# Kernel tuning notes

Measured on AMD Instinct MI355X. Metric: run time of the kernel, lower is better.

## Reference

```python
import jax, jax.numpy as jnp
import numpy as np

T_END = 100.0
EPS = 1e-10
N_MC = 15
BATCH, MAXLEN, HIDDEN = 16, 384, 128


def _mlp(x, W1, b1, W2, b2, W3, b3, W4, b4):
    # x: [..., 1] -> [..., 1]; three tanh hidden layers + softplus head
    h = jnp.tanh(x @ W1 + b1)
    h = jnp.tanh(h @ W2 + b2)
    h = jnp.tanh(h @ W3 + b3)
    return jax.nn.softplus(h @ W4 + b4)


def setup_inputs() -> dict:
    key = jax.random.key(0)
    ks = jax.random.split(key, 6)
    # sorted event times in [0, T_END], zero-padded past seq_len
    times = jnp.sort(jax.random.uniform(ks[0], (BATCH, MAXLEN)) * T_END, axis=1)
    seq_lens = jax.random.randint(ks[1], (BATCH,), 1, MAXLEN + 1)
    valid = jnp.arange(MAXLEN)[None, :] < seq_lens[:, None]
    seq_pads = jnp.where(valid, times, 0.0)[..., None]

    def lin(k, fi, fo):
        bound = 1.0 / np.sqrt(fi)
        kw, kb = jax.random.split(k)
        W = jax.random.uniform(kw, (fi, fo), minval=-bound, maxval=bound)
        b = jax.random.uniform(kb, (fo,), minval=-bound, maxval=bound)
        return W, b

    W1, b1 = lin(ks[2], 1, HIDDEN)
    W2, b2 = lin(ks[3], HIDDEN, HIDDEN)
    W3, b3 = lin(ks[4], HIDDEN, HIDDEN)
    W4, b4 = lin(ks[5], HIDDEN, 1)
    background = jnp.ones((1,))
    return {"seq_pads": seq_pads, "seq_lens": seq_lens, "background": background,
            "W1": W1, "b1": b1, "W2": W2, "b2": b2,
            "W3": W3, "b3": b3, "W4": W4, "b4": b4}


def reference(seq_pads, seq_lens, background, W1, b1, W2, b2, W3, b3, W4, b4):
    batch, maxlen, _ = seq_pads.shape
    t = seq_pads[..., 0]                                   # [B, L]
    # all strictly-lower-triangular pair differences t_i - t_j (j < i), static indices
    r, c = np.tril_indices(maxlen - 1)
    i_idx = r + 1                                          # event index i in 1..L-1
    diffs = t[:, i_idx] - t[:, c]                          # [B, P], P = L*(L-1)/2
    lamb_pairs = _mlp(diffs[..., None], W1, b1, W2, b2, W3, b3, W4, b4)[..., 0]  # [B, P]
    # sum over j < i for each i -> lambs[b, i]; i = 0 gets 0
    lambs = jax.ops.segment_sum(lamb_pairs.T, jnp.asarray(i_idx), num_segments=maxlen).T
    lambs = lambs + background                             # [B, L]

    valid = jnp.arange(maxlen)[None, :] < seq_lens[:, None]
    diff_last = jnp.where(valid, T_END - t, 0.0)           # [B, L]

    # Monte Carlo integral of f over [t_i, T_END], 15 samples
    u = jax.random.uniform(jax.random.key(42), (N_MC, batch, maxlen))
    rand_time = u * diff_last                              # [S, B, L]
    lamb_samples = _mlp(rand_time[..., None], W1, b1, W2, b2, W3, b3, W4, b4)[..., 0] + EPS
    lamb_ints = (lamb_samples * diff_last).mean(0).sum(-1) + T_END * background  # [B]

    sum_log = jnp.where(valid, jnp.log(lambs), 0.0).sum()
    nll = -(sum_log - lamb_ints.sum()) / batch
    return nll
```

## Files before the change

### kernel.cpp

```cpp
#include <hip/hip_runtime.h>
#include <math.h>

#define T_END_F 100.0f
#define N_TAB 4096
#define HID 128
#define EVB 8
#define EVW 2
#define NBLK_TAB (N_TAB / EVB)
#define N_MC_TOTAL 92160
#define TF_HALF 46080u
#define FUSED_BLOCKS 512
#define NSLOT 16

__device__ __forceinline__ float softplusf(float z){
  return fmaxf(z, 0.0f) + log1pf(expf(-fabsf(z)));
}

__device__ __forceinline__ unsigned rotl32(unsigned x, unsigned d){
  return (x << d) | (x >> (32u - d));
}

__device__ float threefry_u01(unsigned idx){
  unsigned i0, i1;
  bool second = idx >= TF_HALF;
  if (second){ i0 = idx - TF_HALF; i1 = idx; }
  else       { i0 = idx;           i1 = idx + TF_HALF; }
  const unsigned ks0 = 0u;
  const unsigned ks1 = 42u;
  const unsigned ks2 = 0x1BD11BDAu ^ ks0 ^ ks1;
  unsigned x0 = i0 + ks0;
  unsigned x1 = i1 + ks1;
#define TF_R(r) { x0 += x1; x1 = rotl32(x1, (r)); x1 ^= x0; }
  TF_R(13) TF_R(15) TF_R(26) TF_R(6)
  x0 += ks1; x1 += ks2 + 1u;
  TF_R(17) TF_R(29) TF_R(16) TF_R(24)
  x0 += ks2; x1 += ks0 + 2u;
  TF_R(13) TF_R(15) TF_R(26) TF_R(6)
  x0 += ks0; x1 += ks1 + 3u;
  TF_R(17) TF_R(29) TF_R(16) TF_R(24)
  x0 += ks1; x1 += ks2 + 4u;
  TF_R(13) TF_R(15) TF_R(26) TF_R(6)
  x0 += ks2; x1 += ks0 + 5u;
#undef TF_R
  unsigned bits = second ? x1 : x0;
  unsigned fb = (bits >> 9) | 0x3F800000u;
  return __uint_as_float(fb) - 1.0f;
}

__device__ __forceinline__ float table_f(const float* __restrict__ tab, float x){
  float pos = x * ((float)(N_TAB - 1) / T_END_F);
  int i = (int)pos;
  if (i < 0) i = 0;
  if (i > N_TAB - 2) i = N_TAB - 2;
  float fr = pos - (float)i;
  float a = tab[i];
  float b = tab[i + 1];
  return fmaf(fr, b - a, a);
}

__device__ __forceinline__ void dense_tanh_layer(
    const float (*__restrict__ hin)[HID], float (*__restrict__ hout)[HID],
    const float* __restrict__ W, const float* __restrict__ bv,
    int k0, int k1, int ebase)
{
  float acc0[EVW], acc1[EVW];
  {
    float ba = bv[k0], bb = bv[k1];
#pragma unroll
    for (int e = 0; e < EVW; ++e){ acc0[e] = ba; acc1[e] = bb; }
  }
#pragma unroll 4
  for (int j = 0; j < HID; j += 4){
    float wa0 = W[(j+0)*HID + k0];
    float wa1 = W[(j+1)*HID + k0];
    float wa2 = W[(j+2)*HID + k0];
    float wa3 = W[(j+3)*HID + k0];
    float wb0 = W[(j+0)*HID + k1];
    float wb1 = W[(j+1)*HID + k1];
    float wb2 = W[(j+2)*HID + k1];
    float wb3 = W[(j+3)*HID + k1];
#pragma unroll
    for (int e = 0; e < EVW; ++e){
      float4 h = *(const float4*)&hin[ebase + e][j];
      float a0 = acc0[e], a1 = acc1[e];
      a0 = fmaf(h.x, wa0, a0); a1 = fmaf(h.x, wb0, a1);
      a0 = fmaf(h.y, wa1, a0); a1 = fmaf(h.y, wb1, a1);
      a0 = fmaf(h.z, wa2, a0); a1 = fmaf(h.z, wb2, a1);
      a0 = fmaf(h.w, wa3, a0); a1 = fmaf(h.w, wb3, a1);
      acc0[e] = a0; acc1[e] = a1;
    }
  }
#pragma unroll
  for (int e = 0; e < EVW; ++e){
    hout[ebase + e][k0] = tanhf(acc0[e]);
    hout[ebase + e][k1] = tanhf(acc1[e]);
  }
}

__global__ __launch_bounds__(256) void build_table_kernel(
    const float* __restrict__ W1, const float* __restrict__ b1v,
    const float* __restrict__ W2, const float* __restrict__ b2v,
    const float* __restrict__ W3, const float* __restrict__ b3v,
    const float* __restrict__ W4, const float* __restrict__ b4v,
    float* __restrict__ tab, float* __restrict__ slots, int* __restrict__ cnt)
{
  __shared__ float hA[EVB][HID];
  __shared__ float hB[EVB][HID];
  const int tid  = threadIdx.x;
  const int wv   = tid >> 6;
  const int lane = tid & 63;
  const int k0 = lane, k1 = lane + 64;
  const int ebase = wv * EVW;
  const int base = blockIdx.x * EVB;
  const float dt = T_END_F / (float)(N_TAB - 1);

  if (blockIdx.x == 0 && tid < 2 * NSLOT + 1){
    if (tid < 2 * NSLOT) slots[tid] = 0.0f;
    else *cnt = 0;
  }

  {
    float wa = W1[k0], wb = W1[k1];
    float ba = b1v[k0], bb = b1v[k1];
#pragma unroll
    for (int e = 0; e < EVW; ++e){
      float x = (float)(base + ebase + e) * dt;
      hA[ebase + e][k0] = tanhf(fmaf(x, wa, ba));
      hA[ebase + e][k1] = tanhf(fmaf(x, wb, bb));
    }
  }
  dense_tanh_layer(hA, hB, W2, b2v, k0, k1, ebase);
  dense_tanh_layer(hB, hA, W3, b3v, k0, k1, ebase);
  {
    float wa = W4[k0], wb = W4[k1];
    float b4s = b4v[0];
#pragma unroll
    for (int e = 0; e < EVW; ++e){
      float p = hA[ebase + e][k0] * wa + hA[ebase + e][k1] * wb;
      p += __shfl_xor(p, 32);
      p += __shfl_xor(p, 16);
      p += __shfl_xor(p, 8);
      p += __shfl_xor(p, 4);
      p += __shfl_xor(p, 2);
      p += __shfl_xor(p, 1);
      if (lane == 0) tab[base + ebase + e] = softplusf(p + b4s);
    }
  }
}

__global__ __launch_bounds__(256) void fused_kernel(
    const float* __restrict__ t,
    const int* __restrict__ seq_lens,
    const float* __restrict__ bg,
    const float* __restrict__ tab,
    float* __restrict__ slots,
    int* __restrict__ cnt,
    float* __restrict__ out)
{
  const int tid  = threadIdx.x;
  const int lane = tid & 63;
  const int wv   = tid >> 6;
  const int gwave = blockIdx.x * 4 + wv;
  const float bgv = bg[0];

  float logsum = 0.0f;
  float mcv    = 0.0f;

#pragma unroll
  for (int k = 0; k < 3; ++k){
    unsigned task = (unsigned)gwave + (unsigned)k * 2048u;
    unsigned b = task / 384u;
    int i = (int)(task - b * 384u);
    if (i < seq_lens[b]){
      const float* tb = t + b * 384u;
      float ti = tb[i];
      float s = 0.0f;
      for (int j = lane; j < i; j += 64)
        s += table_f(tab, ti - tb[j]);
      s += __shfl_xor(s, 32);
      s += __shfl_xor(s, 16);
      s += __shfl_xor(s, 8);
      s += __shfl_xor(s, 4);
      s += __shfl_xor(s, 2);
      s += __shfl_xor(s, 1);
      if (lane == 0) logsum += logf(s + bgv);
    }
  }

  {
    int idx = blockIdx.x * 256 + tid;
    if (idx < N_MC_TOTAL){
      int l = idx % 384;
      int b = (idx / 384) & 15;
      if (l < seq_lens[b]){
        float tv = t[b * 384 + l];
        float dl = T_END_F - tv;
        float u  = threefry_u01((unsigned)idx);
        mcv = (table_f(tab, u * dl) + 1e-10f) * dl;
      }
    }
  }
  mcv += __shfl_xor(mcv, 32);
  mcv += __shfl_xor(mcv, 16);
  mcv += __shfl_xor(mcv, 8);
  mcv += __shfl_xor(mcv, 4);
  mcv += __shfl_xor(mcv, 2);
  mcv += __shfl_xor(mcv, 1);

  __shared__ float redL[4], redM[4];
  if (lane == 0){ redL[wv] = logsum; redM[wv] = mcv; }
  __syncthreads();
  if (tid == 0){
    float bl = redL[0] + redL[1] + redL[2] + redL[3];
    float bm = redM[0] + redM[1] + redM[2] + redM[3];
    int slot = blockIdx.x & (NSLOT - 1);
    atomicAdd(&slots[slot], bl);
    atomicAdd(&slots[NSLOT + slot], bm);
    __threadfence();
    int old = atomicAdd(cnt, 1);
    if (old == (int)gridDim.x - 1){
      float sl = 0.0f, sm = 0.0f;
      for (int q = 0; q < NSLOT; ++q){
        sl += atomicAdd(&slots[q], 0.0f);
        sm += atomicAdd(&slots[NSLOT + q], 0.0f);
      }
      float lamb_ints_total = sm * (1.0f / 15.0f) + 16.0f * T_END_F * bgv;
      out[0] = -(sl - lamb_ints_total) / 16.0f;
    }
  }
}

extern "C" void kernel_launch(void* const* d_in, const int* in_sizes, int n_in,
                              void* d_out, int out_size, void* d_ws, size_t ws_size,
                              hipStream_t stream)
{
  const float* seq_pads = (const float*)d_in[0];
  const int*   seq_lens = (const int*)d_in[1];
  const float* bg       = (const float*)d_in[2];
  const float* W1 = (const float*)d_in[3];
  const float* b1 = (const float*)d_in[4];
  const float* W2 = (const float*)d_in[5];
  const float* b2 = (const float*)d_in[6];
  const float* W3 = (const float*)d_in[7];
  const float* b3 = (const float*)d_in[8];
  const float* W4 = (const float*)d_in[9];
  const float* b4 = (const float*)d_in[10];
  float* out = (float*)d_out;

  float* tab   = (float*)d_ws;
  float* slots = tab + N_TAB;
  int*   cnt   = (int*)(slots + 2 * NSLOT);

  build_table_kernel<<<NBLK_TAB, 256, 0, stream>>>(W1, b1, W2, b2, W3, b3, W4, b4,
                                                   tab, slots, cnt);
  fused_kernel<<<FUSED_BLOCKS, 256, 0, stream>>>(seq_pads, seq_lens, bg, tab,
                                                 slots, cnt, out);
}
```

Baseline: 112.9 us.

## Fuse table build and NLL evaluation into one cooperative kernel with LDS table

Merges the MLP table-building kernel and the pair-sum/Monte Carlo kernel into a single cooperative launch, separated by a grid-wide sync. After the sync each block copies the 4096-entry table into shared memory, and interpolation lookups read from LDS instead of global memory. The aim is to remove one kernel launch boundary and the global-memory gather latency. The cost is a grid-sync barrier and 16KB+ more LDS per block, and it relies on all 512 blocks being co-resident. If the cooperative launch fails, it falls back to the old two-kernel path.

```diff
diff --git a/kernel.cpp b/kernel.cpp
--- a/kernel.cpp
+++ b/kernel.cpp
@@ -1,5 +1,8 @@
 #include <hip/hip_runtime.h>
+#include <hip/hip_cooperative_groups.h>
 #include <math.h>
+
+namespace cg = cooperative_groups;
 
 #define T_END_F 100.0f
 #define N_TAB 4096
@@ -58,6 +61,16 @@
   return fmaf(fr, b - a, a);
 }
 
+#define TABLE_LDS(xval) ({                                        \
+  float _pos = (xval) * ((float)(N_TAB - 1) / T_END_F);           \
+  int _i = (int)_pos;                                             \
+  if (_i < 0) _i = 0;                                             \
+  if (_i > N_TAB - 2) _i = N_TAB - 2;                             \
+  float _fr = _pos - (float)_i;                                   \
+  float _a = sm_tab[_i];                                          \
+  float _b = sm_tab[_i + 1];                                      \
+  fmaf(_fr, _b - _a, _a); })
+
 __device__ __forceinline__ void dense_tanh_layer(
     const float (*__restrict__ hin)[HID], float (*__restrict__ hout)[HID],
     const float* __restrict__ W, const float* __restrict__ bv,
@@ -94,6 +107,145 @@
   for (int e = 0; e < EVW; ++e){
     hout[ebase + e][k0] = tanhf(acc0[e]);
     hout[ebase + e][k1] = tanhf(acc1[e]);
+  }
+}
+
+__global__ __launch_bounds__(256) void mc_nll_fused(
+    const float* __restrict__ W1, const float* __restrict__ b1v,
+    const float* __restrict__ W2, const float* __restrict__ b2v,
+    const float* __restrict__ W3, const float* __restrict__ b3v,
+    const float* __restrict__ W4, const float* __restrict__ b4v,
+    const float* __restrict__ t,
+    const int* __restrict__ seq_lens,
+    const float* __restrict__ bg,
+    float* __restrict__ tab,
+    float* __restrict__ slots,
+    int* __restrict__ cnt,
+    float* __restrict__ out)
+{
+  __shared__ float hA[EVB][HID];
+  __shared__ float hB[EVB][HID];
+  __shared__ float sm_tab[N_TAB];
+  __shared__ float redL[4], redM[4];
+
+  const int tid  = threadIdx.x;
+  const int wv   = tid >> 6;
+  const int lane = tid & 63;
+  const int k0 = lane, k1 = lane + 64;
+  const int ebase = wv * EVW;
+  const int base = blockIdx.x * EVB;
+  const float dt = T_END_F / (float)(N_TAB - 1);
+
+  if (blockIdx.x == 0 && tid < 2 * NSLOT + 1){
+    if (tid < 2 * NSLOT) slots[tid] = 0.0f;
+    else *cnt = 0;
+  }
+
+  {
+    float wa = W1[k0], wb = W1[k1];
+    float ba = b1v[k0], bb = b1v[k1];
+#pragma unroll
+    for (int e = 0; e < EVW; ++e){
+      float x = (float)(base + ebase + e) * dt;
+      hA[ebase + e][k0] = tanhf(fmaf(x, wa, ba));
+      hA[ebase + e][k1] = tanhf(fmaf(x, wb, bb));
+    }
+  }
+  dense_tanh_layer(hA, hB, W2, b2v, k0, k1, ebase);
+  dense_tanh_layer(hB, hA, W3, b3v, k0, k1, ebase);
+  {
+    float wa = W4[k0], wb = W4[k1];
+    float b4s = b4v[0];
+#pragma unroll
+    for (int e = 0; e < EVW; ++e){
+      float p = hA[ebase + e][k0] * wa + hA[ebase + e][k1] * wb;
+      p += __shfl_xor(p, 32);
+      p += __shfl_xor(p, 16);
+      p += __shfl_xor(p, 8);
+      p += __shfl_xor(p, 4);
+      p += __shfl_xor(p, 2);
+      p += __shfl_xor(p, 1);
+      if (lane == 0) tab[base + ebase + e] = softplusf(p + b4s);
+    }
+  }
+
+  cg::this_grid().sync();
+
+  {
+    const float4* g4 = (const float4*)tab;
+    float4* s4 = (float4*)sm_tab;
+#pragma unroll
+    for (int q = 0; q < (N_TAB / 4) / 256; ++q)
+      s4[q * 256 + tid] = g4[q * 256 + tid];
+  }
+  __syncthreads();
+
+  const float bgv = bg[0];
+  const int gwave = blockIdx.x * 4 + wv;
+
+  float logsum = 0.0f;
+  float mcv    = 0.0f;
+
+#pragma unroll
+  for (int k = 0; k < 3; ++k){
+    unsigned task = (unsigned)gwave + (unsigned)k * 2048u;
+    unsigned b = task / 384u;
+    int i = (int)(task - b * 384u);
+    if (i < seq_lens[b]){
+      const float* tb = t + b * 384u;
+      float ti = tb[i];
+      float s = 0.0f;
+      for (int j = lane; j < i; j += 64)
+        s += TABLE_LDS(ti - tb[j]);
+      s += __shfl_xor(s, 32);
+      s += __shfl_xor(s, 16);
+      s += __shfl_xor(s, 8);
+      s += __shfl_xor(s, 4);
+      s += __shfl_xor(s, 2);
+      s += __shfl_xor(s, 1);
+      if (lane == 0) logsum += logf(s + bgv);
+    }
+  }
+
+  {
+    int idx = blockIdx.x * 256 + tid;
+    if (idx < N_MC_TOTAL){
+      int l = idx % 384;
+      int b = (idx / 384) & 15;
+      if (l < seq_lens[b]){
+        float tv = t[b * 384 + l];
+        float dl = T_END_F - tv;
+        float u  = threefry_u01((unsigned)idx);
+        mcv = (TABLE_LDS(u * dl) + 1e-10f) * dl;
+      }
+    }
+  }
+  mcv += __shfl_xor(mcv, 32);
+  mcv += __shfl_xor(mcv, 16);
+  mcv += __shfl_xor(mcv, 8);
+  mcv += __shfl_xor(mcv, 4);
+  mcv += __shfl_xor(mcv, 2);
+  mcv += __shfl_xor(mcv, 1);
+
+  if (lane == 0){ redL[wv] = logsum; redM[wv] = mcv; }
+  __syncthreads();
+  if (tid == 0){
+    float bl = redL[0] + redL[1] + redL[2] + redL[3];
+    float bm = redM[0] + redM[1] + redM[2] + redM[3];
+    int slot = blockIdx.x & (NSLOT - 1);
+    atomicAdd(&slots[slot], bl);
+    atomicAdd(&slots[NSLOT + slot], bm);
+    __threadfence();
+    int old = atomicAdd(cnt, 1);
+    if (old == (int)gridDim.x - 1){
+      float sl = 0.0f, sm = 0.0f;
+      for (int q = 0; q < NSLOT; ++q){
+        sl += atomicAdd(&slots[q], 0.0f);
+        sm += atomicAdd(&slots[NSLOT + q], 0.0f);
+      }
+      float lamb_ints_total = sm * (1.0f / 15.0f) + 16.0f * T_END_F * bgv;
+      out[0] = -(sl - lamb_ints_total) / 16.0f;
+    }
   }
 }
 
@@ -251,8 +403,19 @@
   float* slots = tab + N_TAB;
   int*   cnt   = (int*)(slots + 2 * NSLOT);
 
-  build_table_kernel<<<NBLK_TAB, 256, 0, stream>>>(W1, b1, W2, b2, W3, b3, W4, b4,
-                                                   tab, slots, cnt);
-  fused_kernel<<<FUSED_BLOCKS, 256, 0, stream>>>(seq_pads, seq_lens, bg, tab,
-                                                 slots, cnt, out);
-}
+  void* args[] = {
+    (void*)&W1, (void*)&b1, (void*)&W2, (void*)&b2,
+    (void*)&W3, (void*)&b3, (void*)&W4, (void*)&b4,
+    (void*)&seq_pads, (void*)&seq_lens, (void*)&bg,
+    (void*)&tab, (void*)&slots, (void*)&cnt, (void*)&out
+  };
+  hipError_t err = hipLaunchCooperativeKernel(
+      reinterpret_cast<void*>(mc_nll_fused), dim3(FUSED_BLOCKS), dim3(256),
+      args, 0, stream);
+  if (err != hipSuccess){
+    build_table_kernel<<<NBLK_TAB, 256, 0, stream>>>(W1, b1, W2, b2, W3, b3, W4, b4,
+                                                     tab, slots, cnt);
+    fused_kernel<<<FUSED_BLOCKS, 256, 0, stream>>>(seq_pads, seq_lens, bg, tab,
+                                                   slots, cnt, out);
+  }
+}
```

New measurement: 162.4 us. 1.44x slower.

## Restructure table build, stage lookup table in LDS, spread fused work across more blocks

Applied to the files above, without the earlier changes.

The table-building kernel now uses 512-thread blocks covering 4 events each, with one hidden unit per thread and block barriers between layers. Before, each wave computed two units for two events. The fused kernel copies the 4096-entry table into shared memory once per block, so lookups read from LDS instead of global memory. It also launches 1536 blocks with one pair-sum task per wave instead of three per wave. The intent is more parallelism and cheaper table lookups. The cost is a 16 KB LDS copy per block, extra barriers, and more blocks taking part in the atomic reduction.

```diff
diff --git a/kernel.cpp b/kernel.cpp
--- a/kernel.cpp
+++ b/kernel.cpp
@@ -4,13 +4,15 @@
 #define T_END_F 100.0f
 #define N_TAB 4096
 #define HID 128
-#define EVB 8
-#define EVW 2
-#define NBLK_TAB (N_TAB / EVB)
 #define N_MC_TOTAL 92160
 #define TF_HALF 46080u
-#define FUSED_BLOCKS 512
 #define NSLOT 16
+
+#define B_EV 4
+#define B_THREADS 512
+#define NBLK_BUILD (N_TAB / B_EV)
+
+#define FUSED_BLOCKS 1536
 
 __device__ __forceinline__ float softplusf(float z){
   return fmaxf(z, 0.0f) + log1pf(expf(-fabsf(z)));
@@ -47,71 +49,46 @@
   return __uint_as_float(fb) - 1.0f;
 }
 
-__device__ __forceinline__ float table_f(const float* __restrict__ tab, float x){
-  float pos = x * ((float)(N_TAB - 1) / T_END_F);
-  int i = (int)pos;
-  if (i < 0) i = 0;
-  if (i > N_TAB - 2) i = N_TAB - 2;
-  float fr = pos - (float)i;
-  float a = tab[i];
-  float b = tab[i + 1];
-  return fmaf(fr, b - a, a);
-}
-
-__device__ __forceinline__ void dense_tanh_layer(
-    const float (*__restrict__ hin)[HID], float (*__restrict__ hout)[HID],
-    const float* __restrict__ W, const float* __restrict__ bv,
-    int k0, int k1, int ebase)
-{
-  float acc0[EVW], acc1[EVW];
-  {
-    float ba = bv[k0], bb = bv[k1];
-#pragma unroll
-    for (int e = 0; e < EVW; ++e){ acc0[e] = ba; acc1[e] = bb; }
-  }
+#define TABLE_LDS(xval) ({                                        \
+  float _pos = (xval) * ((float)(N_TAB - 1) / T_END_F);           \
+  int _i = (int)_pos;                                             \
+  if (_i < 0) _i = 0;                                             \
+  if (_i > N_TAB - 2) _i = N_TAB - 2;                             \
+  float _fr = _pos - (float)_i;                                   \
+  float _a = sm_tab[_i];                                          \
+  float _b = sm_tab[_i + 1];                                      \
+  fmaf(_fr, _b - _a, _a); })
+
+__device__ __forceinline__ float dense_dot(
+    const float* __restrict__ hrow,
+    const float* __restrict__ W,
+    int k, float bias)
+{
+  float acc = bias;
 #pragma unroll 4
   for (int j = 0; j < HID; j += 4){
-    float wa0 = W[(j+0)*HID + k0];
-    float wa1 = W[(j+1)*HID + k0];
-    float wa2 = W[(j+2)*HID + k0];
-    float wa3 = W[(j+3)*HID + k0];
-    float wb0 = W[(j+0)*HID + k1];
-    float wb1 = W[(j+1)*HID + k1];
-    float wb2 = W[(j+2)*HID + k1];
-    float wb3 = W[(j+3)*HID + k1];
-#pragma unroll
-    for (int e = 0; e < EVW; ++e){
-      float4 h = *(const float4*)&hin[ebase + e][j];
-      float a0 = acc0[e], a1 = acc1[e];
-      a0 = fmaf(h.x, wa0, a0); a1 = fmaf(h.x, wb0, a1);
-      a0 = fmaf(h.y, wa1, a0); a1 = fmaf(h.y, wb1, a1);
-      a0 = fmaf(h.z, wa2, a0); a1 = fmaf(h.z, wb2, a1);
-      a0 = fmaf(h.w, wa3, a0); a1 = fmaf(h.w, wb3, a1);
-      acc0[e] = a0; acc1[e] = a1;
-    }
-  }
-#pragma unroll
-  for (int e = 0; e < EVW; ++e){
-    hout[ebase + e][k0] = tanhf(acc0[e]);
-    hout[ebase + e][k1] = tanhf(acc1[e]);
-  }
-}
-
-__global__ __launch_bounds__(256) void build_table_kernel(
+    float4 h = *(const float4*)&hrow[j];
+    acc = fmaf(h.x, W[(j+0)*HID + k], acc);
+    acc = fmaf(h.y, W[(j+1)*HID + k], acc);
+    acc = fmaf(h.z, W[(j+2)*HID + k], acc);
+    acc = fmaf(h.w, W[(j+3)*HID + k], acc);
+  }
+  return acc;
+}
+
+__global__ __launch_bounds__(B_THREADS) void build_table_kernel(
     const float* __restrict__ W1, const float* __restrict__ b1v,
     const float* __restrict__ W2, const float* __restrict__ b2v,
     const float* __restrict__ W3, const float* __restrict__ b3v,
     const float* __restrict__ W4, const float* __restrict__ b4v,
     float* __restrict__ tab, float* __restrict__ slots, int* __restrict__ cnt)
 {
-  __shared__ float hA[EVB][HID];
-  __shared__ float hB[EVB][HID];
-  const int tid  = threadIdx.x;
-  const int wv   = tid >> 6;
-  const int lane = tid & 63;
-  const int k0 = lane, k1 = lane + 64;
-  const int ebase = wv * EVW;
-  const int base = blockIdx.x * EVB;
+  __shared__ float hA[B_EV][HID];
+  __shared__ float hB[B_EV][HID];
+  const int tid = threadIdx.x;
+  const int e   = tid >> 7;
+  const int k   = tid & 127;
+  const int base = blockIdx.x * B_EV;
   const float dt = T_END_F / (float)(N_TAB - 1);
 
   if (blockIdx.x == 0 && tid < 2 * NSLOT + 1){
@@ -120,30 +97,32 @@
   }
 
   {
-    float wa = W1[k0], wb = W1[k1];
-    float ba = b1v[k0], bb = b1v[k1];
-#pragma unroll
-    for (int e = 0; e < EVW; ++e){
-      float x = (float)(base + ebase + e) * dt;
-      hA[ebase + e][k0] = tanhf(fmaf(x, wa, ba));
-      hA[ebase + e][k1] = tanhf(fmaf(x, wb, bb));
-    }
-  }
-  dense_tanh_layer(hA, hB, W2, b2v, k0, k1, ebase);
-  dense_tanh_layer(hB, hA, W3, b3v, k0, k1, ebase);
-  {
-    float wa = W4[k0], wb = W4[k1];
-    float b4s = b4v[0];
-#pragma unroll
-    for (int e = 0; e < EVW; ++e){
-      float p = hA[ebase + e][k0] * wa + hA[ebase + e][k1] * wb;
+    float x = (float)(base + e) * dt;
+    hA[e][k] = tanhf(fmaf(x, W1[k], b1v[k]));
+  }
+  __syncthreads();
+
+  hB[e][k] = tanhf(dense_dot(hA[e], W2, k, b2v[k]));
+  __syncthreads();
+
+  hA[e][k] = tanhf(dense_dot(hB[e], W3, k, b3v[k]));
+  __syncthreads();
+
+  {
+    const int wv   = tid >> 6;
+    const int lane = tid & 63;
+    if ((wv & 1) == 0){
+      const int ee = wv >> 1;
+      float wa = W4[lane], wb = W4[lane + 64];
+      float b4s = b4v[0];
+      float p = hA[ee][lane] * wa + hA[ee][lane + 64] * wb;
       p += __shfl_xor(p, 32);
       p += __shfl_xor(p, 16);
       p += __shfl_xor(p, 8);
       p += __shfl_xor(p, 4);
       p += __shfl_xor(p, 2);
       p += __shfl_xor(p, 1);
-      if (lane == 0) tab[base + ebase + e] = softplusf(p + b4s);
+      if (lane == 0) tab[base + ee] = softplusf(p + b4s);
     }
   }
 }
@@ -157,18 +136,28 @@
     int* __restrict__ cnt,
     float* __restrict__ out)
 {
+  __shared__ float sm_tab[N_TAB];
+  __shared__ float redL[4], redM[4];
+
   const int tid  = threadIdx.x;
   const int lane = tid & 63;
   const int wv   = tid >> 6;
-  const int gwave = blockIdx.x * 4 + wv;
   const float bgv = bg[0];
+
+  {
+    const float4* g4 = (const float4*)tab;
+    float4* s4 = (float4*)sm_tab;
+#pragma unroll
+    for (int q = 0; q < 4; ++q)
+      s4[q * 256 + tid] = g4[q * 256 + tid];
+  }
+  __syncthreads();
 
   float logsum = 0.0f;
   float mcv    = 0.0f;
 
-#pragma unroll
-  for (int k = 0; k < 3; ++k){
-    unsigned task = (unsigned)gwave + (unsigned)k * 2048u;
+  {
+    unsigned task = (unsigned)(blockIdx.x * 4 + wv);
     unsigned b = task / 384u;
     int i = (int)(task - b * 384u);
     if (i < seq_lens[b]){
@@ -176,14 +165,14 @@
       float ti = tb[i];
       float s = 0.0f;
       for (int j = lane; j < i; j += 64)
-        s += table_f(tab, ti - tb[j]);
+        s += TABLE_LDS(ti - tb[j]);
       s += __shfl_xor(s, 32);
       s += __shfl_xor(s, 16);
       s += __shfl_xor(s, 8);
       s += __shfl_xor(s, 4);
       s += __shfl_xor(s, 2);
       s += __shfl_xor(s, 1);
-      if (lane == 0) logsum += logf(s + bgv);
+      if (lane == 0) logsum = logf(s + bgv);
     }
   }
 
@@ -196,7 +185,7 @@
         float tv = t[b * 384 + l];
         float dl = T_END_F - tv;
         float u  = threefry_u01((unsigned)idx);
-        mcv = (table_f(tab, u * dl) + 1e-10f) * dl;
+        mcv = (TABLE_LDS(u * dl) + 1e-10f) * dl;
       }
     }
   }
@@ -207,7 +196,6 @@
   mcv += __shfl_xor(mcv, 2);
   mcv += __shfl_xor(mcv, 1);
 
-  __shared__ float redL[4], redM[4];
   if (lane == 0){ redL[wv] = logsum; redM[wv] = mcv; }
   __syncthreads();
   if (tid == 0){
@@ -251,8 +239,8 @@
   float* slots = tab + N_TAB;
   int*   cnt   = (int*)(slots + 2 * NSLOT);
 
-  build_table_kernel<<<NBLK_TAB, 256, 0, stream>>>(W1, b1, W2, b2, W3, b3, W4, b4,
-                                                   tab, slots, cnt);
-  fused_kernel<<<FUSED_BLOCKS, 256, 0, stream>>>(seq_pads, seq_lens, bg, tab,
-                                                 slots, cnt, out);
-}
+  build_table_kernel<<<NBLK_BUILD, B_THREADS, 0, stream>>>(
+      W1, b1, W2, b2, W3, b3, W4, b4, tab, slots, cnt);
+  fused_kernel<<<FUSED_BLOCKS, 256, 0, stream>>>(
+      seq_pads, seq_lens, bg, tab, slots, cnt, out);
+}
```

After: 136.5 us. +20.9%, slower.
